# Optimization experiments

Hardware: AMD Instinct MI355X
Metric: run time of the kernel (lower is better)

## Reference

```python
import jax, jax.numpy as jnp
import numpy as np

ROUTING_ITERS = 3
EPS = 1e-9


def squash(s):
    # s: [..., D]; faithful to the torch code: x / (1 + n^2) / sqrt(n^2 + eps)
    sq = jnp.sum(s * s, axis=-1, keepdims=True)
    return s / (1.0 + sq) / jnp.sqrt(sq + EPS)


def setup_inputs() -> dict:
    key = jax.random.key(0)
    k1, k2 = jax.random.split(key)
    B, I, C, D, d = 64, 4096, 32, 16, 16
    x = jax.random.normal(k1, (B, I, d), dtype=jnp.float32)
    weights = jax.random.normal(k2, (1, I, C, D, d), dtype=jnp.float32)
    return {"x": x, "weights": weights}


def reference(x, weights):
    # u_hat[b,i,c,D] = weights[0,i,c,D,d] @ x[b,i,d]
    u_hat = jnp.einsum('icDd,bid->bicD', weights[0], x)  # [B, I, C, D]
    B, I, C, D = u_hat.shape
    b_ij = jnp.zeros((B, I, C), dtype=u_hat.dtype)
    v_j = None
    for _ in range(ROUTING_ITERS):
        c_ij = jax.nn.softmax(b_ij, axis=2)                     # [B, I, C]
        s_j = jnp.einsum('bic,bicD->bcD', c_ij, u_hat)          # [B, C, D]
        v_j = squash(s_j)                                       # [B, C, D]
        b_ij = b_ij + jnp.einsum('bicD,bcD->bic', u_hat, v_j)   # agreement
    return v_j
```

## Files before the change

### kernel.cpp

```cpp
#include <hip/hip_runtime.h>
#include <math.h>

#define ITILES 256
#define IPB    16

typedef __bf16 bf16x8 __attribute__((ext_vector_type(8)));
typedef float  f32x16 __attribute__((ext_vector_type(16)));

__device__ inline unsigned short f2bf(float f) {
    unsigned int x = __float_as_uint(f);
    x += 0x7fff + ((x >> 16) & 1);
    return (unsigned short)(x >> 16);
}
__device__ inline float bf2f(unsigned short u) {
    return __uint_as_float(((unsigned int)u) << 16);
}
__device__ inline uint4 pack8(const unsigned short* o) {
    uint4 p;
    p.x = o[0] | ((unsigned)o[1] << 16);
    p.y = o[2] | ((unsigned)o[3] << 16);
    p.z = o[4] | ((unsigned)o[5] << 16);
    p.w = o[6] | ((unsigned)o[7] << 16);
    return p;
}

__device__ inline unsigned cvtpk(float lo, float hi) {
    unsigned r;
    asm("v_cvt_pk_bf16_f32 %0, %1, %2" : "=v"(r) : "v"(lo), "v"(hi));
    return r;
}
__device__ inline unsigned split3(float x, float y, unsigned& q2, unsigned& q3) {
    unsigned q1 = cvtpk(x, y);
    float f1x = __uint_as_float(q1 << 16);
    float f1y = __uint_as_float(q1 & 0xffff0000u);
    float rx = x - f1x, ry = y - f1y;
    q2 = cvtpk(rx, ry);
    float f2x = __uint_as_float(q2 << 16);
    float f2y = __uint_as_float(q2 & 0xffff0000u);
    q3 = cvtpk(rx - f2x, ry - f2y);
    return q1;
}

__global__ __launch_bounds__(128) void prep_x(const float* __restrict__ x,
                                              unsigned short* __restrict__ Xp)
{
    const int i = blockIdx.x;
    const int t = threadIdx.x;
    const int b = t >> 1, kh = t & 1;
    const float4* s4 = (const float4*)(x + ((size_t)b * 4096 + i) * 16 + kh * 8);
    float4 wa = s4[0], wb = s4[1];
    float wv[8] = {wa.x, wa.y, wa.z, wa.w, wb.x, wb.y, wb.z, wb.w};
    unsigned short o1[8], o2[8], o3[8];
    #pragma unroll
    for (int j = 0; j < 8; ++j) {
        float w = wv[j];
        o1[j] = f2bf(w);            float f1 = bf2f(o1[j]);
        o2[j] = f2bf(w - f1);       float f2 = bf2f(o2[j]);
        o3[j] = f2bf(w - f1 - f2);
    }
    unsigned short* dst = Xp + (size_t)i * 3072 + kh * 1536 + b * 8;
    *(uint4*)(dst)        = pack8(o1);
    *(uint4*)(dst + 512)  = pack8(o2);
    *(uint4*)(dst + 1024) = pack8(o3);
}

#define MF(A_, B_, C_) __builtin_amdgcn_mfma_f32_32x32x16_bf16( \
    __builtin_bit_cast(bf16x8, A_), __builtin_bit_cast(bf16x8, B_), C_, 0, 0, 0)

__global__ __launch_bounds__(256, 5)
void pass0_kernel(const float* __restrict__ W,
                  const unsigned short* __restrict__ Xp,
                  float* __restrict__ slab)
{
    const int tid   = threadIdx.x;
    const int lane  = tid & 63;
    const int l31   = lane & 31;
    const int h     = lane >> 5;
    const int bid   = blockIdx.x;
    const int itile = bid >> 2;
    const int mt    = ((bid & 3) << 2) + (tid >> 6);
    const int cA    = 2 * mt + h;
    const int i0    = itile * IPB;

    const int cW = 2 * mt + ((l31 >> 2) & 1);
    const int DW = (l31 & 3) + 4 * (l31 >> 3);
    const float4* w4 = (const float4*)(W + (size_t)i0 * 8192 + ((cW * 16 + DW) * 16 + h * 8));

    f32x16 s0, s1;
    #pragma unroll
    for (int q = 0; q < 16; ++q) { s0[q] = 0.f; s1[q] = 0.f; }

    float4 wa = w4[0], wb = w4[1];

    for (int ii = 0; ii < IPB; ++ii) {
        const int i = i0 + ii;
        const unsigned short* bb = Xp + (size_t)i * 3072 + (size_t)h * 1536 + l31 * 8;

        uint4 a1, a2, a3;
        a1.x = split3(wa.x, wa.y, a2.x, a3.x);
        a1.y = split3(wa.z, wa.w, a2.y, a3.y);
        a1.z = split3(wb.x, wb.y, a2.z, a3.z);
        a1.w = split3(wb.z, wb.w, a2.w, a3.w);

        {
            const int iin = (ii + 1 < IPB) ? (ii + 1) : ii;
            wa = w4[(size_t)iin * 2048];
            wb = w4[(size_t)iin * 2048 + 1];
        }

        #pragma unroll
        for (int nt = 0; nt < 2; ++nt) {
            const unsigned short* bp = bb + nt * 256;
            f32x16& ss = nt ? s1 : s0;
            uint4 b1 = *(const uint4*)(bp);
            uint4 b2 = *(const uint4*)(bp + 512);
            ss = MF(a1, b1, ss);
            ss = MF(a2, b1, ss);
            uint4 b3 = *(const uint4*)(bp + 1024);
            ss = MF(a1, b2, ss);
            ss = MF(a3, b1, ss);
            ss = MF(a2, b2, ss);
            ss = MF(a1, b3, ss);
        }
    }

    float4* slab4 = (float4*)slab;
    #pragma unroll
    for (int nt = 0; nt < 2; ++nt) {
        const f32x16& ss = nt ? s1 : s0;
        const int b = nt * 32 + l31;
        size_t base = ((size_t)itile * 64 + b) * 128 + cA * 4;
        #pragma unroll
        for (int dblk = 0; dblk < 4; ++dblk) {
            float4 o = {ss[dblk * 4 + 0], ss[dblk * 4 + 1], ss[dblk * 4 + 2], ss[dblk * 4 + 3]};
            slab4[base + dblk] = o;
        }
    }
}

__global__ __launch_bounds__(1024, 4)
void pass1_kernel(const float* __restrict__ W,
                  const unsigned short* __restrict__ Xp,
                  const float* __restrict__ vg,
                  float* __restrict__ slab)
{
    __shared__ float4 vt[8192];
    __shared__ float  p_lds[32 * 65];
    __shared__ float  cij_lds[32 * 65];

    const int tid   = threadIdx.x;
    const int mt    = tid >> 6;
    const int lane  = tid & 63;
    const int l31   = lane & 31;
    const int h     = lane >> 5;
    const int cA    = 2 * mt + h;
    const int itile = blockIdx.x;
    const int i0    = itile * IPB;

    const int cW = 2 * mt + ((l31 >> 2) & 1);
    const int DW = (l31 & 3) + 4 * (l31 >> 3);
    const float4* w4 = (const float4*)(W + (size_t)i0 * 8192 + ((cW * 16 + DW) * 16 + h * 8));

    {
        const float4* v4 = (const float4*)vg;
        #pragma unroll
        for (int k = 0; k < 8; ++k) {
            int idx = k * 1024 + tid;
            int b = idx >> 7, cd = idx & 127;
            vt[b * 128 + (cd ^ (b & 31))] = v4[idx];
        }
        __syncthreads();
    }

    f32x16 s0, s1;
    #pragma unroll
    for (int q = 0; q < 16; ++q) { s0[q] = 0.f; s1[q] = 0.f; }

    float4 wa0 = w4[0],    wb0 = w4[1];
    float4 wa1 = w4[2048], wb1 = w4[2049];

    for (int ii = 0; ii < IPB; ++ii) {
        const int i = i0 + ii;
        const unsigned short* bb = Xp + (size_t)i * 3072 + (size_t)h * 1536 + l31 * 8;

        uint4 a1, a2, a3;
        a1.x = split3(wa0.x, wa0.y, a2.x, a3.x);
        a1.y = split3(wa0.z, wa0.w, a2.y, a3.y);
        a1.z = split3(wb0.x, wb0.y, a2.z, a3.z);
        a1.w = split3(wb0.z, wb0.w, a2.w, a3.w);

        wa0 = wa1; wb0 = wb1;
        {
            const int iin = (ii + 2 < IPB) ? (ii + 2) : (IPB - 1);
            wa1 = w4[(size_t)iin * 2048];
            wb1 = w4[(size_t)iin * 2048 + 1];
        }

        #pragma unroll
        for (int nt = 0; nt < 2; ++nt) {
            const unsigned short* bp = bb + nt * 256;
            uint4 b1 = *(const uint4*)(bp);
            uint4 b2 = *(const uint4*)(bp + 512);
            uint4 b3 = *(const uint4*)(bp + 1024);

            f32x16 u;
            #pragma unroll
            for (int q = 0; q < 16; ++q) u[q] = 0.f;
            __builtin_amdgcn_s_setprio(1);
            u = MF(a1, b1, u);
            u = MF(a2, b1, u);
            u = MF(a1, b2, u);
            u = MF(a3, b1, u);
            u = MF(a2, b2, u);
            u = MF(a1, b3, u);
            __builtin_amdgcn_s_setprio(0);

            const int b = nt * 32 + l31;
            float p = 0.f;
            #pragma unroll
            for (int dblk = 0; dblk < 4; ++dblk) {
                float4 vv = vt[b * 128 + ((cA * 4 + dblk) ^ l31)];
                p = fmaf(u[dblk * 4 + 0], vv.x, p);
                p = fmaf(u[dblk * 4 + 1], vv.y, p);
                p = fmaf(u[dblk * 4 + 2], vv.z, p);
                p = fmaf(u[dblk * 4 + 3], vv.w, p);
            }
            p_lds[cA * 65 + b] = p;
            __syncthreads();

            {
                const int bsm = nt * 32 + mt * 2 + h;
                float e = __expf(p_lds[l31 * 65 + bsm]);
                float t = e;
                t += __shfl_xor(t, 16); t += __shfl_xor(t, 8);
                t += __shfl_xor(t, 4);  t += __shfl_xor(t, 2);
                t += __shfl_xor(t, 1);
                cij_lds[l31 * 65 + bsm] = __fdividef(e, t);
            }
            __syncthreads();

            {
                f32x16& ss = nt ? s1 : s0;
                const float cij = cij_lds[cA * 65 + b];
                #pragma unroll
                for (int q = 0; q < 16; ++q) ss[q] = fmaf(cij, u[q], ss[q]);
            }
        }
    }

    float4* slab4 = (float4*)slab;
    #pragma unroll
    for (int nt = 0; nt < 2; ++nt) {
        const f32x16& ss = nt ? s1 : s0;
        const int b = nt * 32 + l31;
        size_t base = ((size_t)itile * 64 + b) * 128 + cA * 4;
        #pragma unroll
        for (int dblk = 0; dblk < 4; ++dblk) {
            float4 o = {ss[dblk * 4 + 0], ss[dblk * 4 + 1], ss[dblk * 4 + 2], ss[dblk * 4 + 3]};
            slab4[base + dblk] = o;
        }
    }
}
#undef MF

__global__ __launch_bounds__(256)
void reduce_squash(const float* __restrict__ slab, float* __restrict__ out, float scale,
                   const float* __restrict__ v1in, float* __restrict__ vsum)
{
    __shared__ float part[7][32];
    const int tid = threadIdx.x;
    const int q   = tid >> 5;
    const int ol  = tid & 31;
    const int o   = blockIdx.x * 32 + ol;
    float a[8];
    #pragma unroll
    for (int k = 0; k < 8; ++k) a[k] = 0.f;
    #pragma unroll
    for (int g = 0; g < 4; ++g) {
        #pragma unroll
        for (int k = 0; k < 8; ++k)
            a[k] += slab[(size_t)(q * 32 + g * 8 + k) * 32768 + o];
    }
    float s = 0.f;
    #pragma unroll
    for (int k = 0; k < 8; ++k) s += a[k];
    if (q) part[q - 1][ol] = s;
    __syncthreads();
    if (q == 0) {
        #pragma unroll
        for (int j = 0; j < 7; ++j) s += part[j][ol];
        s *= scale;
        float t = s * s;
        t += __shfl_xor(t, 1);
        t += __shfl_xor(t, 2);
        t += __shfl_xor(t, 4);
        t += __shfl_xor(t, 8);
        float r = s / (1.0f + t) / sqrtf(t + 1e-9f);
        out[o] = r;
        if (v1in) vsum[o] = r + v1in[o];
    }
}

extern "C" void kernel_launch(void* const* d_in, const int* in_sizes, int n_in,
                              void* d_out, int out_size, void* d_ws, size_t ws_size,
                              hipStream_t stream)
{
    const float* x = (const float*)d_in[0];
    const float* W = (const float*)d_in[1];

    float* slab = (float*)d_ws;
    float* v1   = slab + (size_t)ITILES * 32768;
    float* v2   = v1 + 32768;
    float* v12  = v2 + 32768;
    unsigned short* Xp = (unsigned short*)(v12 + 32768);
    float* out  = (float*)d_out;

    hipLaunchKernelGGL(prep_x, dim3(4096), dim3(128), 0, stream, x, Xp);

    hipLaunchKernelGGL(pass0_kernel,  dim3(1024), dim3(256),  0, stream, W, Xp, slab);
    hipLaunchKernelGGL(reduce_squash, dim3(1024), dim3(256),  0, stream, slab, v1, 1.0f / 32.0f, (const float*)nullptr, (float*)nullptr);
    hipLaunchKernelGGL(pass1_kernel,  dim3(ITILES), dim3(1024), 0, stream, W, Xp, v1, slab);
    hipLaunchKernelGGL(reduce_squash, dim3(1024), dim3(256),  0, stream, slab, v2, 1.0f, v1, v12);
    hipLaunchKernelGGL(pass1_kernel,  dim3(ITILES), dim3(1024), 0, stream, W, Xp, v12, slab);
    hipLaunchKernelGGL(reduce_squash, dim3(1024), dim3(256),  0, stream, slab, out, 1.0f, (const float*)nullptr, (float*)nullptr);
}
```

Baseline: 375.8 us.

## Fuse all routing passes into one cooperative persistent kernel with grid syncs

Replaces the seven launches (x prep, pass0, three reductions, two routing passes) with a single cooperative kernel of 256 blocks. Grid-wide syncs separate the phases. The x bf16 split is done per tile and also staged in LDS for pass 0. Reductions are spread across the same 256 blocks. This removes launch gaps and the separate prep pass. In exchange, pass 0 now runs with 1024-thread blocks instead of the earlier 1024 blocks of 256 threads, and each grid sync adds barrier cost.

```diff
diff --git a/kernel.cpp b/kernel.cpp
--- a/kernel.cpp
+++ b/kernel.cpp
@@ -1,5 +1,8 @@
 #include <hip/hip_runtime.h>
+#include <hip/hip_cooperative_groups.h>
 #include <math.h>
+
+namespace cg = cooperative_groups;
 
 #define ITILES 256
 #define IPB    16
@@ -23,7 +26,6 @@
     p.w = o[6] | ((unsigned)o[7] << 16);
     return p;
 }
-
 __device__ inline unsigned cvtpk(float lo, float hi) {
     unsigned r;
     asm("v_cvt_pk_bf16_f32 %0, %1, %2" : "=v"(r) : "v"(lo), "v"(hi));
@@ -41,112 +43,24 @@
     return q1;
 }
 
-__global__ __launch_bounds__(128) void prep_x(const float* __restrict__ x,
-                                              unsigned short* __restrict__ Xp)
-{
-    const int i = blockIdx.x;
-    const int t = threadIdx.x;
-    const int b = t >> 1, kh = t & 1;
-    const float4* s4 = (const float4*)(x + ((size_t)b * 4096 + i) * 16 + kh * 8);
-    float4 wa = s4[0], wb = s4[1];
-    float wv[8] = {wa.x, wa.y, wa.z, wa.w, wb.x, wb.y, wb.z, wb.w};
-    unsigned short o1[8], o2[8], o3[8];
-    #pragma unroll
-    for (int j = 0; j < 8; ++j) {
-        float w = wv[j];
-        o1[j] = f2bf(w);            float f1 = bf2f(o1[j]);
-        o2[j] = f2bf(w - f1);       float f2 = bf2f(o2[j]);
-        o3[j] = f2bf(w - f1 - f2);
-    }
-    unsigned short* dst = Xp + (size_t)i * 3072 + kh * 1536 + b * 8;
-    *(uint4*)(dst)        = pack8(o1);
-    *(uint4*)(dst + 512)  = pack8(o2);
-    *(uint4*)(dst + 1024) = pack8(o3);
-}
-
 #define MF(A_, B_, C_) __builtin_amdgcn_mfma_f32_32x32x16_bf16( \
     __builtin_bit_cast(bf16x8, A_), __builtin_bit_cast(bf16x8, B_), C_, 0, 0, 0)
 
-__global__ __launch_bounds__(256, 5)
-void pass0_kernel(const float* __restrict__ W,
-                  const unsigned short* __restrict__ Xp,
-                  float* __restrict__ slab)
-{
-    const int tid   = threadIdx.x;
-    const int lane  = tid & 63;
-    const int l31   = lane & 31;
-    const int h     = lane >> 5;
-    const int bid   = blockIdx.x;
-    const int itile = bid >> 2;
-    const int mt    = ((bid & 3) << 2) + (tid >> 6);
-    const int cA    = 2 * mt + h;
-    const int i0    = itile * IPB;
-
-    const int cW = 2 * mt + ((l31 >> 2) & 1);
-    const int DW = (l31 & 3) + 4 * (l31 >> 3);
-    const float4* w4 = (const float4*)(W + (size_t)i0 * 8192 + ((cW * 16 + DW) * 16 + h * 8));
-
-    f32x16 s0, s1;
-    #pragma unroll
-    for (int q = 0; q < 16; ++q) { s0[q] = 0.f; s1[q] = 0.f; }
-
-    float4 wa = w4[0], wb = w4[1];
-
-    for (int ii = 0; ii < IPB; ++ii) {
-        const int i = i0 + ii;
-        const unsigned short* bb = Xp + (size_t)i * 3072 + (size_t)h * 1536 + l31 * 8;
-
-        uint4 a1, a2, a3;
-        a1.x = split3(wa.x, wa.y, a2.x, a3.x);
-        a1.y = split3(wa.z, wa.w, a2.y, a3.y);
-        a1.z = split3(wb.x, wb.y, a2.z, a3.z);
-        a1.w = split3(wb.z, wb.w, a2.w, a3.w);
-
-        {
-            const int iin = (ii + 1 < IPB) ? (ii + 1) : ii;
-            wa = w4[(size_t)iin * 2048];
-            wb = w4[(size_t)iin * 2048 + 1];
-        }
-
-        #pragma unroll
-        for (int nt = 0; nt < 2; ++nt) {
-            const unsigned short* bp = bb + nt * 256;
-            f32x16& ss = nt ? s1 : s0;
-            uint4 b1 = *(const uint4*)(bp);
-            uint4 b2 = *(const uint4*)(bp + 512);
-            ss = MF(a1, b1, ss);
-            ss = MF(a2, b1, ss);
-            uint4 b3 = *(const uint4*)(bp + 1024);
-            ss = MF(a1, b2, ss);
-            ss = MF(a3, b1, ss);
-            ss = MF(a2, b2, ss);
-            ss = MF(a1, b3, ss);
-        }
-    }
-
-    float4* slab4 = (float4*)slab;
-    #pragma unroll
-    for (int nt = 0; nt < 2; ++nt) {
-        const f32x16& ss = nt ? s1 : s0;
-        const int b = nt * 32 + l31;
-        size_t base = ((size_t)itile * 64 + b) * 128 + cA * 4;
-        #pragma unroll
-        for (int dblk = 0; dblk < 4; ++dblk) {
-            float4 o = {ss[dblk * 4 + 0], ss[dblk * 4 + 1], ss[dblk * 4 + 2], ss[dblk * 4 + 3]};
-            slab4[base + dblk] = o;
-        }
-    }
-}
-
 __global__ __launch_bounds__(1024, 4)
-void pass1_kernel(const float* __restrict__ W,
-                  const unsigned short* __restrict__ Xp,
-                  const float* __restrict__ vg,
-                  float* __restrict__ slab)
+void mega_kernel(const float* __restrict__ W,
+                 const float* __restrict__ x,
+                 unsigned short* __restrict__ Xp,
+                 float* __restrict__ slab,
+                 float* __restrict__ v1,
+                 float* __restrict__ v2,
+                 float* __restrict__ v12,
+                 float* __restrict__ out)
 {
     __shared__ float4 vt[8192];
     __shared__ float  p_lds[32 * 65];
     __shared__ float  cij_lds[32 * 65];
+
+    cg::grid_group grid = cg::this_grid();
 
     const int tid   = threadIdx.x;
     const int mt    = tid >> 6;
@@ -157,149 +71,246 @@
     const int itile = blockIdx.x;
     const int i0    = itile * IPB;
 
+    {
+        unsigned short* XpL = (unsigned short*)vt;
+        const int il = tid >> 6;
+        const int bb = tid & 63;
+        const float4* s4 = (const float4*)(x + ((size_t)bb * 4096 + (i0 + il)) * 16);
+        #pragma unroll
+        for (int kh = 0; kh < 2; ++kh) {
+            float4 xa = s4[kh * 2], xb = s4[kh * 2 + 1];
+            float wv[8] = {xa.x, xa.y, xa.z, xa.w, xb.x, xb.y, xb.z, xb.w};
+            unsigned short o1[8], o2[8], o3[8];
+            #pragma unroll
+            for (int j = 0; j < 8; ++j) {
+                float w = wv[j];
+                o1[j] = f2bf(w);            float f1 = bf2f(o1[j]);
+                o2[j] = f2bf(w - f1);       float f2 = bf2f(o2[j]);
+                o3[j] = f2bf(w - f1 - f2);
+            }
+            uint4 q1 = pack8(o1), q2 = pack8(o2), q3 = pack8(o3);
+            const size_t off = (size_t)il * 3072 + kh * 1536 + bb * 8;
+            unsigned short* g = Xp + (size_t)i0 * 3072 + off;
+            *(uint4*)(g)          = q1;
+            *(uint4*)(g + 512)    = q2;
+            *(uint4*)(g + 1024)   = q3;
+            unsigned short* l = XpL + off;
+            *(uint4*)(l)          = q1;
+            *(uint4*)(l + 512)    = q2;
+            *(uint4*)(l + 1024)   = q3;
+        }
+    }
+    __syncthreads();
+
     const int cW = 2 * mt + ((l31 >> 2) & 1);
     const int DW = (l31 & 3) + 4 * (l31 >> 3);
     const float4* w4 = (const float4*)(W + (size_t)i0 * 8192 + ((cW * 16 + DW) * 16 + h * 8));
 
+    auto slab_write = [&](const f32x16& s0, const f32x16& s1) {
+        float4* slab4 = (float4*)slab;
+        #pragma unroll
+        for (int nt = 0; nt < 2; ++nt) {
+            const f32x16& ss = nt ? s1 : s0;
+            const int b = nt * 32 + l31;
+            size_t base = ((size_t)itile * 64 + b) * 128 + cA * 4;
+            #pragma unroll
+            for (int dblk = 0; dblk < 4; ++dblk) {
+                float4 o = {ss[dblk*4+0], ss[dblk*4+1], ss[dblk*4+2], ss[dblk*4+3]};
+                slab4[base + dblk] = o;
+            }
+        }
+    };
+
+    auto do_reduce = [&](float* dst, float scale,
+                         const float* v1in, float* vsum) {
+        float* part = p_lds;
+        const int sub = tid >> 7;
+        const int ol  = tid & 127;
+        const int o   = itile * 128 + ol;
+        float a[8];
+        #pragma unroll
+        for (int k = 0; k < 8; ++k) a[k] = 0.f;
+        #pragma unroll
+        for (int g = 0; g < 4; ++g) {
+            #pragma unroll
+            for (int k = 0; k < 8; ++k)
+                a[k] += slab[(size_t)(sub * 32 + g * 8 + k) * 32768 + o];
+        }
+        float s = 0.f;
+        #pragma unroll
+        for (int k = 0; k < 8; ++k) s += a[k];
+        if (sub) part[(sub - 1) * 128 + ol] = s;
+        __syncthreads();
+        if (sub == 0) {
+            #pragma unroll
+            for (int j = 0; j < 7; ++j) s += part[j * 128 + ol];
+            s *= scale;
+            float t = s * s;
+            t += __shfl_xor(t, 1);
+            t += __shfl_xor(t, 2);
+            t += __shfl_xor(t, 4);
+            t += __shfl_xor(t, 8);
+            float r = s / (1.0f + t) / sqrtf(t + 1e-9f);
+            dst[o] = r;
+            if (v1in) vsum[o] = r + v1in[o];
+        }
+        __syncthreads();
+    };
+
     {
-        const float4* v4 = (const float4*)vg;
-        #pragma unroll
-        for (int k = 0; k < 8; ++k) {
-            int idx = k * 1024 + tid;
-            int b = idx >> 7, cd = idx & 127;
-            vt[b * 128 + (cd ^ (b & 31))] = v4[idx];
-        }
-        __syncthreads();
+        const unsigned short* XpL = (const unsigned short*)vt;
+        f32x16 s0, s1;
+        #pragma unroll
+        for (int q = 0; q < 16; ++q) { s0[q] = 0.f; s1[q] = 0.f; }
+
+        float4 wa0 = w4[0],    wb0 = w4[1];
+        float4 wa1 = w4[2048], wb1 = w4[2049];
+
+        for (int ii = 0; ii < IPB; ++ii) {
+            const unsigned short* bl = XpL + (size_t)ii * 3072 + (size_t)h * 1536 + l31 * 8;
+
+            uint4 a1, a2, a3;
+            a1.x = split3(wa0.x, wa0.y, a2.x, a3.x);
+            a1.y = split3(wa0.z, wa0.w, a2.y, a3.y);
+            a1.z = split3(wb0.x, wb0.y, a2.z, a3.z);
+            a1.w = split3(wb0.z, wb0.w, a2.w, a3.w);
+
+            wa0 = wa1; wb0 = wb1;
+            {
+                const int iin = (ii + 2 < IPB) ? (ii + 2) : (IPB - 1);
+                wa1 = w4[(size_t)iin * 2048];
+                wb1 = w4[(size_t)iin * 2048 + 1];
+            }
+
+            #pragma unroll
+            for (int nt = 0; nt < 2; ++nt) {
+                const unsigned short* bp = bl + nt * 256;
+                f32x16& ss = nt ? s1 : s0;
+                uint4 b1 = *(const uint4*)(bp);
+                uint4 b2 = *(const uint4*)(bp + 512);
+                uint4 b3 = *(const uint4*)(bp + 1024);
+                __builtin_amdgcn_s_setprio(1);
+                ss = MF(a1, b1, ss);
+                ss = MF(a2, b1, ss);
+                ss = MF(a1, b2, ss);
+                ss = MF(a3, b1, ss);
+                ss = MF(a2, b2, ss);
+                ss = MF(a1, b3, ss);
+                __builtin_amdgcn_s_setprio(0);
+            }
+        }
+        slab_write(s0, s1);
     }
-
-    f32x16 s0, s1;
-    #pragma unroll
-    for (int q = 0; q < 16; ++q) { s0[q] = 0.f; s1[q] = 0.f; }
-
-    float4 wa0 = w4[0],    wb0 = w4[1];
-    float4 wa1 = w4[2048], wb1 = w4[2049];
-
-    for (int ii = 0; ii < IPB; ++ii) {
-        const int i = i0 + ii;
-        const unsigned short* bb = Xp + (size_t)i * 3072 + (size_t)h * 1536 + l31 * 8;
-
-        uint4 a1, a2, a3;
-        a1.x = split3(wa0.x, wa0.y, a2.x, a3.x);
-        a1.y = split3(wa0.z, wa0.w, a2.y, a3.y);
-        a1.z = split3(wb0.x, wb0.y, a2.z, a3.z);
-        a1.w = split3(wb0.z, wb0.w, a2.w, a3.w);
-
-        wa0 = wa1; wb0 = wb1;
+    __threadfence();
+    grid.sync();
+
+    do_reduce(v1, 1.0f / 32.0f, nullptr, nullptr);
+    __threadfence();
+    grid.sync();
+
+    auto pass1_phase = [&](const float* vg) {
         {
-            const int iin = (ii + 2 < IPB) ? (ii + 2) : (IPB - 1);
-            wa1 = w4[(size_t)iin * 2048];
-            wb1 = w4[(size_t)iin * 2048 + 1];
-        }
-
-        #pragma unroll
-        for (int nt = 0; nt < 2; ++nt) {
-            const unsigned short* bp = bb + nt * 256;
-            uint4 b1 = *(const uint4*)(bp);
-            uint4 b2 = *(const uint4*)(bp + 512);
-            uint4 b3 = *(const uint4*)(bp + 1024);
-
-            f32x16 u;
-            #pragma unroll
-            for (int q = 0; q < 16; ++q) u[q] = 0.f;
-            __builtin_amdgcn_s_setprio(1);
-            u = MF(a1, b1, u);
-            u = MF(a2, b1, u);
-            u = MF(a1, b2, u);
-            u = MF(a3, b1, u);
-            u = MF(a2, b2, u);
-            u = MF(a1, b3, u);
-            __builtin_amdgcn_s_setprio(0);
-
-            const int b = nt * 32 + l31;
-            float p = 0.f;
-            #pragma unroll
-            for (int dblk = 0; dblk < 4; ++dblk) {
-                float4 vv = vt[b * 128 + ((cA * 4 + dblk) ^ l31)];
-                p = fmaf(u[dblk * 4 + 0], vv.x, p);
-                p = fmaf(u[dblk * 4 + 1], vv.y, p);
-                p = fmaf(u[dblk * 4 + 2], vv.z, p);
-                p = fmaf(u[dblk * 4 + 3], vv.w, p);
-            }
-            p_lds[cA * 65 + b] = p;
+            const float4* v4 = (const float4*)vg;
+            #pragma unroll
+            for (int k = 0; k < 8; ++k) {
+                int idx = k * 1024 + tid;
+                int b = idx >> 7, cd = idx & 127;
+                vt[b * 128 + (cd ^ (b & 31))] = v4[idx];
+            }
             __syncthreads();
-
+        }
+
+        f32x16 s0, s1;
+        #pragma unroll
+        for (int q = 0; q < 16; ++q) { s0[q] = 0.f; s1[q] = 0.f; }
+
+        float4 wa0 = w4[0],    wb0 = w4[1];
+        float4 wa1 = w4[2048], wb1 = w4[2049];
+
+        for (int ii = 0; ii < IPB; ++ii) {
+            const int i = i0 + ii;
+            const unsigned short* bb = Xp + (size_t)i * 3072 + (size_t)h * 1536 + l31 * 8;
+
+            uint4 a1, a2, a3;
+            a1.x = split3(wa0.x, wa0.y, a2.x, a3.x);
+            a1.y = split3(wa0.z, wa0.w, a2.y, a3.y);
+            a1.z = split3(wb0.x, wb0.y, a2.z, a3.z);
+            a1.w = split3(wb0.z, wb0.w, a2.w, a3.w);
+
+            wa0 = wa1; wb0 = wb1;
             {
-                const int bsm = nt * 32 + mt * 2 + h;
-                float e = __expf(p_lds[l31 * 65 + bsm]);
-                float t = e;
-                t += __shfl_xor(t, 16); t += __shfl_xor(t, 8);
-                t += __shfl_xor(t, 4);  t += __shfl_xor(t, 2);
-                t += __shfl_xor(t, 1);
-                cij_lds[l31 * 65 + bsm] = __fdividef(e, t);
-            }
-            __syncthreads();
-
-            {
-                f32x16& ss = nt ? s1 : s0;
-                const float cij = cij_lds[cA * 65 + b];
+                const int iin = (ii + 2 < IPB) ? (ii + 2) : (IPB - 1);
+                wa1 = w4[(size_t)iin * 2048];
+                wb1 = w4[(size_t)iin * 2048 + 1];
+            }
+
+            #pragma unroll
+            for (int nt = 0; nt < 2; ++nt) {
+                const unsigned short* bp = bb + nt * 256;
+                uint4 b1 = *(const uint4*)(bp);
+                uint4 b2 = *(const uint4*)(bp + 512);
+                uint4 b3 = *(const uint4*)(bp + 1024);
+
+                f32x16 u;
                 #pragma unroll
-                for (int q = 0; q < 16; ++q) ss[q] = fmaf(cij, u[q], ss[q]);
-            }
-        }
-    }
-
-    float4* slab4 = (float4*)slab;
-    #pragma unroll
-    for (int nt = 0; nt < 2; ++nt) {
-        const f32x16& ss = nt ? s1 : s0;
-        const int b = nt * 32 + l31;
-        size_t base = ((size_t)itile * 64 + b) * 128 + cA * 4;
-        #pragma unroll
-        for (int dblk = 0; dblk < 4; ++dblk) {
-            float4 o = {ss[dblk * 4 + 0], ss[dblk * 4 + 1], ss[dblk * 4 + 2], ss[dblk * 4 + 3]};
-            slab4[base + dblk] = o;
-        }
-    }
+                for (int q = 0; q < 16; ++q) u[q] = 0.f;
+                __builtin_amdgcn_s_setprio(1);
+                u = MF(a1, b1, u);
+                u = MF(a2, b1, u);
+                u = MF(a1, b2, u);
+                u = MF(a3, b1, u);
+                u = MF(a2, b2, u);
+                u = MF(a1, b3, u);
+                __builtin_amdgcn_s_setprio(0);
+
+                const int b = nt * 32 + l31;
+                float p = 0.f;
+                #pragma unroll
+                for (int dblk = 0; dblk < 4; ++dblk) {
+                    float4 vv = vt[b * 128 + ((cA * 4 + dblk) ^ l31)];
+                    p = fmaf(u[dblk * 4 + 0], vv.x, p);
+                    p = fmaf(u[dblk * 4 + 1], vv.y, p);
+                    p = fmaf(u[dblk * 4 + 2], vv.z, p);
+                    p = fmaf(u[dblk * 4 + 3], vv.w, p);
+                }
+                p_lds[cA * 65 + b] = p;
+                __syncthreads();
+
+                {
+                    const int bsm = nt * 32 + mt * 2 + h;
+                    float e = __expf(p_lds[l31 * 65 + bsm]);
+                    float t = e;
+                    t += __shfl_xor(t, 16); t += __shfl_xor(t, 8);
+                    t += __shfl_xor(t, 4);  t += __shfl_xor(t, 2);
+                    t += __shfl_xor(t, 1);
+                    cij_lds[l31 * 65 + bsm] = __fdividef(e, t);
+                }
+                __syncthreads();
+
+                {
+                    f32x16& ss = nt ? s1 : s0;
+                    const float cij = cij_lds[cA * 65 + b];
+                    #pragma unroll
+                    for (int q = 0; q < 16; ++q) ss[q] = fmaf(cij, u[q], ss[q]);
+                }
+            }
+        }
+        slab_write(s0, s1);
+    };
+
+    pass1_phase(v1);
+    __threadfence();
+    grid.sync();
+    do_reduce(v2, 1.0f, v1, v12);
+    __threadfence();
+    grid.sync();
+
+    pass1_phase(v12);
+    __threadfence();
+    grid.sync();
+    do_reduce(out, 1.0f, nullptr, nullptr);
 }
 #undef MF
-
-__global__ __launch_bounds__(256)
-void reduce_squash(const float* __restrict__ slab, float* __restrict__ out, float scale,
-                   const float* __restrict__ v1in, float* __restrict__ vsum)
-{
-    __shared__ float part[7][32];
-    const int tid = threadIdx.x;
-    const int q   = tid >> 5;
-    const int ol  = tid & 31;
-    const int o   = blockIdx.x * 32 + ol;
-    float a[8];
-    #pragma unroll
-    for (int k = 0; k < 8; ++k) a[k] = 0.f;
-    #pragma unroll
-    for (int g = 0; g < 4; ++g) {
-        #pragma unroll
-        for (int k = 0; k < 8; ++k)
-            a[k] += slab[(size_t)(q * 32 + g * 8 + k) * 32768 + o];
-    }
-    float s = 0.f;
-    #pragma unroll
-    for (int k = 0; k < 8; ++k) s += a[k];
-    if (q) part[q - 1][ol] = s;
-    __syncthreads();
-    if (q == 0) {
-        #pragma unroll
-        for (int j = 0; j < 7; ++j) s += part[j][ol];
-        s *= scale;
-        float t = s * s;
-        t += __shfl_xor(t, 1);
-        t += __shfl_xor(t, 2);
-        t += __shfl_xor(t, 4);
-        t += __shfl_xor(t, 8);
-        float r = s / (1.0f + t) / sqrtf(t + 1e-9f);
-        out[o] = r;
-        if (v1in) vsum[o] = r + v1in[o];
-    }
-}
 
 extern "C" void kernel_launch(void* const* d_in, const int* in_sizes, int n_in,
                               void* d_out, int out_size, void* d_ws, size_t ws_size,
@@ -315,12 +326,10 @@
     unsigned short* Xp = (unsigned short*)(v12 + 32768);
     float* out  = (float*)d_out;
 
-    hipLaunchKernelGGL(prep_x, dim3(4096), dim3(128), 0, stream, x, Xp);
-
-    hipLaunchKernelGGL(pass0_kernel,  dim3(1024), dim3(256),  0, stream, W, Xp, slab);
-    hipLaunchKernelGGL(reduce_squash, dim3(1024), dim3(256),  0, stream, slab, v1, 1.0f / 32.0f, (const float*)nullptr, (float*)nullptr);
-    hipLaunchKernelGGL(pass1_kernel,  dim3(ITILES), dim3(1024), 0, stream, W, Xp, v1, slab);
-    hipLaunchKernelGGL(reduce_squash, dim3(1024), dim3(256),  0, stream, slab, v2, 1.0f, v1, v12);
-    hipLaunchKernelGGL(pass1_kernel,  dim3(ITILES), dim3(1024), 0, stream, W, Xp, v12, slab);
-    hipLaunchKernelGGL(reduce_squash, dim3(1024), dim3(256),  0, stream, slab, out, 1.0f, (const float*)nullptr, (float*)nullptr);
-}
+    void* args[] = {
+        (void*)&W, (void*)&x, (void*)&Xp, (void*)&slab,
+        (void*)&v1, (void*)&v2, (void*)&v12, (void*)&out
+    };
+    hipLaunchCooperativeKernel((const void*)mega_kernel,
+                               dim3(ITILES), dim3(1024), args, 0, stream);
+}
```

Measured after the change: 1.279 ms. 3.4x slower.
